# Performance work log

Hardware: AMD Instinct MI355X
Metric: run time of the kernel (lower is better)

## Reference

```python
import jax, jax.numpy as jnp
import numpy as np

NF = 51          # num_features = n_queries + 1
UNITS = 128      # rnn_units
LAG = 14
GAMMA = 28
OP_SCALE = 0.05
Q_SCALE = 0.02
C = float(np.log(np.expm1(1.0)))  # softplus shift so softplus(C)=1
OUT = 2 * NF     # DenseVariational units
NW = UNITS * OUT + OUT  # kernel + bias size = 13158


def setup_inputs() -> dict:
    key = jax.random.key(0)
    ks = jax.random.split(key, 6)
    B, T = 8192, 64
    x = jax.random.normal(ks[0], (B, T, NF), dtype=jnp.float32)
    gru_kernel = 0.1 * jax.random.normal(ks[1], (NF, 3 * UNITS), dtype=jnp.float32)
    gru_rkernel = 0.1 * jax.random.normal(ks[2], (UNITS, 3 * UNITS), dtype=jnp.float32)
    gru_bias = 0.05 * jax.random.normal(ks[3], (2, 3 * UNITS), dtype=jnp.float32)
    post_loc = 0.05 * jax.random.normal(ks[4], (NW,), dtype=jnp.float32)
    post_rho = -3.0 + 0.1 * jax.random.normal(ks[5], (NW,), dtype=jnp.float32)
    return {"x": x, "gru_kernel": gru_kernel, "gru_rkernel": gru_rkernel,
            "gru_bias": gru_bias, "post_loc": post_loc, "post_rho": post_rho}


def reference(x, gru_kernel, gru_rkernel, gru_bias, post_loc, post_rho):
    B = x.shape[0]

    def gru_step(h, xt):
        # Keras GRUCell, reset_after=True (dual bias)
        mx = xt @ gru_kernel + gru_bias[0]   # (B, 3U)
        mh = h @ gru_rkernel + gru_bias[1]   # (B, 3U)
        xz, xr, xh = jnp.split(mx, 3, axis=-1)
        rz, rr, rh = jnp.split(mh, 3, axis=-1)
        z = jax.nn.sigmoid(xz + rz)
        r = jax.nn.sigmoid(xr + rr)
        hh = jnp.tanh(xh + r * rh)
        return z * h + (1.0 - z) * hh

    def sample_dv(h, eps_w):
        # DenseVariational: sample flat weight vector from diag-Gaussian posterior
        scale = 1e-5 + Q_SCALE * jax.nn.softplus(C + post_rho)
        w = post_loc + scale * eps_w
        kernel = w[:UNITS * OUT].reshape(UNITS, OUT)
        bias = w[UNITS * OUT:]
        return h @ kernel + bias  # (B, OUT)

    # Deterministic sampling noise (reparameterization)
    nk = jax.random.key(42)
    eps_w = jax.random.normal(jax.random.fold_in(nk, 0), (GAMMA, NW), dtype=jnp.float32)
    eps_s = jax.random.normal(jax.random.fold_in(nk, 1), (GAMMA - 1, B, NF), dtype=jnp.float32)

    # Encoder GRU over inputs[:, :-LAG, :]
    seq = jnp.swapaxes(x[:, :-LAG, :], 0, 1)  # (T', B, NF)
    h0 = jnp.zeros((B, UNITS), dtype=x.dtype)
    h_enc = jax.lax.scan(lambda h, xt: (gru_step(h, xt), None), h0, seq)[0]

    t0 = sample_dv(h_enc, eps_w[0])  # (B, OUT)

    def dec_step(carry, eps):
        h, t = carry
        ew, es = eps
        loc = t[:, :NF]
        sc = 1e-5 + OP_SCALE * jax.nn.softplus(C + t[:, NF:])
        s = loc + sc * es                    # Normal(...).sample()
        h2 = gru_step(h, s)
        t2 = sample_dv(h2, ew)
        return (h2, t2), t2

    _, ts = jax.lax.scan(dec_step, (h_enc, t0), (eps_w[1:], eps_s))  # (GAMMA-1, B, OUT)
    preds = jnp.concatenate([t0[None], ts], axis=0)       # (GAMMA, B, OUT)
    preds = jnp.transpose(preds, (1, 0, 2))               # (B, GAMMA, OUT)

    loc = preds[..., :NF]
    scale = 1e-5 + OP_SCALE * jax.nn.softplus(C + preds[..., NF:])
    return jnp.concatenate([loc, scale], axis=-1)         # (B, GAMMA, 2*NF)
```

## Files before the change

### kernel.cpp

```cpp
#include <hip/hip_runtime.h>
#include <stdint.h>

#define NF 51
#define UNITS 128
#define G3 384
#define OUT_C 102
#define NW 13158
#define GAMMA 28
#define BATCH 8192
#define SEQ_T 64
#define TSTEPS 50
#define NDEC 27
#define BR 32
#define THREADS 1024
#define CCONST 0.5413248546129181f
#define WF_USHORTS 147456
#define WDF_USHORTS 802816
#define WDF_FRAG_THREADS 401408
#define HB_ELEMS 2856

typedef __attribute__((ext_vector_type(8))) short bf16x8;
typedef __attribute__((ext_vector_type(4))) float f32x4;
typedef unsigned short ushort_t;

__host__ __device__ __forceinline__ void tf2x32(uint32_t k0, uint32_t k1,
    uint32_t x0, uint32_t x1, uint32_t& o0, uint32_t& o1)
{
  uint32_t ks2 = k0 ^ k1 ^ 0x1BD11BDAu;
  x0 += k0; x1 += k1;
#define TF_R(r) { x0 += x1; x1 = (x1 << (r)) | (x1 >> (32 - (r))); x1 ^= x0; }
  TF_R(13) TF_R(15) TF_R(26) TF_R(6)  x0 += k1;  x1 += ks2 + 1u;
  TF_R(17) TF_R(29) TF_R(16) TF_R(24) x0 += ks2; x1 += k0 + 2u;
  TF_R(13) TF_R(15) TF_R(26) TF_R(6)  x0 += k0;  x1 += k1 + 3u;
  TF_R(17) TF_R(29) TF_R(16) TF_R(24) x0 += k1;  x1 += ks2 + 4u;
  TF_R(13) TF_R(15) TF_R(26) TF_R(6)  x0 += ks2; x1 += k0 + 5u;
#undef TF_R
  o0 = x0; o1 = x1;
}

__device__ __forceinline__ float erfinv_f(float x) {
  float w = -log1pf(-x * x);
  float p;
  if (w < 5.0f) {
    w -= 2.5f;
    p = 2.81022636e-08f;
    p = fmaf(p, w, 3.43273939e-07f);
    p = fmaf(p, w, -3.5233877e-06f);
    p = fmaf(p, w, -4.39150654e-06f);
    p = fmaf(p, w, 0.00021858087f);
    p = fmaf(p, w, -0.00125372503f);
    p = fmaf(p, w, -0.00417768164f);
    p = fmaf(p, w, 0.246640727f);
    p = fmaf(p, w, 1.50140941f);
  } else {
    w = sqrtf(w) - 3.0f;
    p = -0.000200214257f;
    p = fmaf(p, w, 0.000100950558f);
    p = fmaf(p, w, 0.00134934322f);
    p = fmaf(p, w, -0.00367342844f);
    p = fmaf(p, w, 0.00573950773f);
    p = fmaf(p, w, -0.0076224613f);
    p = fmaf(p, w, 0.00943887047f);
    p = fmaf(p, w, 1.00167406f);
    p = fmaf(p, w, 2.83297682f);
  }
  return p * x;
}

__device__ __forceinline__ float jax_normal(uint32_t k0, uint32_t k1, uint32_t i)
{
  uint32_t y0, y1;
  tf2x32(k0, k1, 0u, i, y0, y1);
  uint32_t bits = y0 ^ y1;
  uint32_t fb = (bits >> 9) | 0x3f800000u;
  float f = __uint_as_float(fb) - 1.0f;
  const float lo = -0.99999994f;
  const float d  = 1.99999994f;
  float u = __fadd_rn(__fmul_rn(f, d), lo);
  u = fmaxf(lo, u);
  return 1.41421354f * erfinv_f(u);
}

__device__ __forceinline__ float softplus_f(float x) {
  return fmaxf(x, 0.0f) + log1pf(expf(-fabsf(x)));
}
__device__ __forceinline__ float rcp_f(float x) { return __builtin_amdgcn_rcpf(x); }
__device__ __forceinline__ float sigmoid_fast(float x) {
  return rcp_f(1.0f + __expf(-x));
}
__device__ __forceinline__ float tanh_fast(float x) {
  return 1.0f - 2.0f * rcp_f(1.0f + __expf(2.0f * x));
}

__device__ __forceinline__ ushort_t f2bf(float f) {
  uint32_t u = __float_as_uint(f);
  uint32_t r = (u + 0x7fffu + ((u >> 16) & 1u)) >> 16;
  return (ushort_t)r;
}
__device__ __forceinline__ float bf2f(ushort_t h) {
  return __uint_as_float(((uint32_t)h) << 16);
}

__global__ void build_wf_kernel(const float* __restrict__ Wh,
                                const float* __restrict__ Wx,
                                ushort_t* __restrict__ wf)
{
  int t = blockIdx.x * 256 + threadIdx.x;
  if (t >= WF_USHORTS) return;
  int e    = t & 7;
  int lane = (t >> 3) & 63;
  int sp   = (t >> 9) & 1;
  int q    = t >> 10;
  int ks   = q % 6;
  int nb   = q / 6;
  int kl   = 8 * (lane >> 4) + e;
  int col  = 16 * nb + (lane & 15);
  float w;
  if (ks < 4) {
    w = Wh[(32 * ks + kl) * G3 + col];
  } else {
    int row = 32 * (ks - 4) + kl;
    w = (row < NF) ? Wx[row * G3 + col] : 0.0f;
  }
  ushort_t hi = f2bf(w);
  wf[t] = (sp == 0) ? hi : f2bf(w - bf2f(hi));
}

__global__ void build_wdf_kernel(const float* __restrict__ post_loc,
                                 const float* __restrict__ post_rho,
                                 ushort_t* __restrict__ wdf,
                                 float* __restrict__ hbias,
                                 uint32_t kw0, uint32_t kw1)
{
  int t = blockIdx.x * 256 + threadIdx.x;
  if (t < WDF_FRAG_THREADS) {
    int e    = t & 7;
    int lane = (t >> 3) & 63;
    int ks   = (t >> 9) & 3;
    int q    = t >> 11;
    int nt   = q % 7;
    int g    = q / 7;
    int k    = 32 * ks + 8 * (lane >> 4) + e;
    int col  = 16 * nt + (lane & 15);
    float w = 0.0f;
    if (col < OUT_C) {
      int widx = k * OUT_C + col;
      float eps = jax_normal(kw0, kw1, (uint32_t)(g * NW + widx));
      float sc = 1e-5f + 0.02f * softplus_f(CCONST + post_rho[widx]);
      w = fmaf(sc, eps, post_loc[widx]);
    }
    ushort_t hi = f2bf(w);
    size_t base = (size_t)(q * 4 + ks) * 1024 + lane * 8 + e;
    wdf[base]       = hi;
    wdf[base + 512] = f2bf(w - bf2f(hi));
  } else if (t < WDF_FRAG_THREADS + HB_ELEMS) {
    int u = t - WDF_FRAG_THREADS;
    int col = u % OUT_C, g = u / OUT_C;
    int widx = UNITS * OUT_C + col;
    float eps = jax_normal(kw0, kw1, (uint32_t)(g * NW + widx));
    float sc = 1e-5f + 0.02f * softplus_f(CCONST + post_rho[widx]);
    hbias[u] = fmaf(sc, eps, post_loc[widx]);
  }
}

__global__ __launch_bounds__(THREADS, 4)
__attribute__((amdgpu_waves_per_eu(4, 4)))
void irnn_main(
    const float* __restrict__ x,
    const float* __restrict__ gbias,
    const ushort_t* __restrict__ WF,
    const ushort_t* __restrict__ WDF,
    const float* __restrict__ HB,
    float* __restrict__ out,
    uint32_t ks0, uint32_t ks1)
{
  __shared__ __align__(16) ushort_t h_hi[BR][136];
  __shared__ __align__(16) ushort_t h_lo[BR][136];
  __shared__ __align__(16) ushort_t s_hi[BR][72];
  __shared__ __align__(16) ushort_t s_lo[BR][72];
  __shared__ float t_lds[BR][OUT_C];

  const int tid  = threadIdx.x;
  const int b0   = blockIdx.x * BR;
  const int lane = tid & 63;
  const int wv   = tid >> 6;
  const int kg   = lane >> 4;
  const int fr   = lane & 15;
  const int g3   = wv >> 1;
  const int rbase = 16 * (wv & 1);
  const int c    = 16 * g3 + fr;

  const float bz  = gbias[c]           + gbias[G3 + c];
  const float brg = gbias[UNITS + c]   + gbias[G3 + UNITS + c];
  const float bxh = gbias[2*UNITS + c];
  const float brh = gbias[G3 + 2*UNITS + c];

  float hreg[4] = {0.f, 0.f, 0.f, 0.f};

  for (int i = tid; i < BR * 136; i += THREADS) { (&h_hi[0][0])[i] = 0; (&h_lo[0][0])[i] = 0; }
  for (int i = tid; i < BR * 72;  i += THREADS) { (&s_hi[0][0])[i] = 0; (&s_lo[0][0])[i] = 0; }
  __syncthreads();

  const ushort_t* wfz = WF + (size_t)g3        * 6144 + (size_t)lane * 8;
  const ushort_t* wfr = WF + (size_t)(8 + g3)  * 6144 + (size_t)lane * 8;
  const ushort_t* wfh = WF + (size_t)(16 + g3) * 6144 + (size_t)lane * 8;

  auto gru_phase = [&]() {
    f32x4 acc_z  = {0.f,0.f,0.f,0.f};
    f32x4 acc_r  = {0.f,0.f,0.f,0.f};
    f32x4 acc_rh = {0.f,0.f,0.f,0.f};
    f32x4 acc_xh = {0.f,0.f,0.f,0.f};
    #pragma unroll 2
    for (int ks = 0; ks < 4; ++ks) {
      const int off = 32*ks + 8*kg;
      bf16x8 ah = *(const bf16x8*)&h_hi[rbase + fr][off];
      bf16x8 al = *(const bf16x8*)&h_lo[rbase + fr][off];
      bf16x8 bh = *(const bf16x8*)(wfz + (2*ks + 0) * 512);
      bf16x8 bl = *(const bf16x8*)(wfz + (2*ks + 1) * 512);
      acc_z = __builtin_amdgcn_mfma_f32_16x16x32_bf16(ah, bh, acc_z, 0,0,0);
      acc_z = __builtin_amdgcn_mfma_f32_16x16x32_bf16(ah, bl, acc_z, 0,0,0);
      acc_z = __builtin_amdgcn_mfma_f32_16x16x32_bf16(al, bh, acc_z, 0,0,0);
      bh = *(const bf16x8*)(wfr + (2*ks + 0) * 512);
      bl = *(const bf16x8*)(wfr + (2*ks + 1) * 512);
      acc_r = __builtin_amdgcn_mfma_f32_16x16x32_bf16(ah, bh, acc_r, 0,0,0);
      acc_r = __builtin_amdgcn_mfma_f32_16x16x32_bf16(ah, bl, acc_r, 0,0,0);
      acc_r = __builtin_amdgcn_mfma_f32_16x16x32_bf16(al, bh, acc_r, 0,0,0);
      bh = *(const bf16x8*)(wfh + (2*ks + 0) * 512);
      bl = *(const bf16x8*)(wfh + (2*ks + 1) * 512);
      acc_rh = __builtin_amdgcn_mfma_f32_16x16x32_bf16(ah, bh, acc_rh, 0,0,0);
      acc_rh = __builtin_amdgcn_mfma_f32_16x16x32_bf16(ah, bl, acc_rh, 0,0,0);
      acc_rh = __builtin_amdgcn_mfma_f32_16x16x32_bf16(al, bh, acc_rh, 0,0,0);
    }
    #pragma unroll 2
    for (int ks = 4; ks < 6; ++ks) {
      const int off = 32*(ks - 4) + 8*kg;
      bf16x8 ah = *(const bf16x8*)&s_hi[rbase + fr][off];
      bf16x8 al = *(const bf16x8*)&s_lo[rbase + fr][off];
      bf16x8 bh = *(const bf16x8*)(wfz + (2*ks + 0) * 512);
      bf16x8 bl = *(const bf16x8*)(wfz + (2*ks + 1) * 512);
      acc_z = __builtin_amdgcn_mfma_f32_16x16x32_bf16(ah, bh, acc_z, 0,0,0);
      acc_z = __builtin_amdgcn_mfma_f32_16x16x32_bf16(ah, bl, acc_z, 0,0,0);
      acc_z = __builtin_amdgcn_mfma_f32_16x16x32_bf16(al, bh, acc_z, 0,0,0);
      bh = *(const bf16x8*)(wfr + (2*ks + 0) * 512);
      bl = *(const bf16x8*)(wfr + (2*ks + 1) * 512);
      acc_r = __builtin_amdgcn_mfma_f32_16x16x32_bf16(ah, bh, acc_r, 0,0,0);
      acc_r = __builtin_amdgcn_mfma_f32_16x16x32_bf16(ah, bl, acc_r, 0,0,0);
      acc_r = __builtin_amdgcn_mfma_f32_16x16x32_bf16(al, bh, acc_r, 0,0,0);
      bh = *(const bf16x8*)(wfh + (2*ks + 0) * 512);
      bl = *(const bf16x8*)(wfh + (2*ks + 1) * 512);
      acc_xh = __builtin_amdgcn_mfma_f32_16x16x32_bf16(ah, bh, acc_xh, 0,0,0);
      acc_xh = __builtin_amdgcn_mfma_f32_16x16x32_bf16(ah, bl, acc_xh, 0,0,0);
      acc_xh = __builtin_amdgcn_mfma_f32_16x16x32_bf16(al, bh, acc_xh, 0,0,0);
    }
    __syncthreads();
    const int orow = rbase + 4 * kg;
    #pragma unroll
    for (int j = 0; j < 4; ++j) {
      float az = acc_z[j]  + bz;
      float ar = acc_r[j]  + brg;
      float rh = acc_rh[j] + brh;
      float xh = acc_xh[j] + bxh;
      float z  = sigmoid_fast(az);
      float rr = sigmoid_fast(ar);
      float hh = tanh_fast(fmaf(rr, rh, xh));
      float h  = z * hreg[j] + (1.0f - z) * hh;
      hreg[j]  = h;
      ushort_t hi = f2bf(h);
      h_hi[orow + j][c] = hi;
      h_lo[orow + j][c] = f2bf(h - bf2f(hi));
    }
  };

  auto head = [&](int g) {
    if (wv < 14) {
      const int nt = wv % 7, mt = wv / 7;
      const ushort_t* WB = WDF + (size_t)(g * 7 + nt) * 4096 + (size_t)lane * 8;
      f32x4 acc = {0.f,0.f,0.f,0.f};
      #pragma unroll 2
      for (int ks = 0; ks < 4; ++ks) {
        const int off = 32*ks + 8*kg;
        bf16x8 ah = *(const bf16x8*)&h_hi[16*mt + fr][off];
        bf16x8 al = *(const bf16x8*)&h_lo[16*mt + fr][off];
        bf16x8 bh = *(const bf16x8*)(WB + (2*ks + 0) * 512);
        bf16x8 bl = *(const bf16x8*)(WB + (2*ks + 1) * 512);
        acc = __builtin_amdgcn_mfma_f32_16x16x32_bf16(ah, bh, acc, 0,0,0);
        acc = __builtin_amdgcn_mfma_f32_16x16x32_bf16(ah, bl, acc, 0,0,0);
        acc = __builtin_amdgcn_mfma_f32_16x16x32_bf16(al, bh, acc, 0,0,0);
      }
      const int col = 16*nt + fr;
      if (col < OUT_C) {
        float kb = HB[g * OUT_C + col];
        const int r0 = 16*mt + 4*kg;
        #pragma unroll
        for (int j = 0; j < 4; ++j) {
          float tv = acc[j] + kb;
          t_lds[r0 + j][col] = tv;
          float ov = (col < NF) ? tv
                               : (1e-5f + 0.05f * softplus_f(CCONST + tv));
          out[(size_t)(b0 + r0 + j) * (GAMMA * OUT_C) + g * OUT_C + col] = ov;
        }
      }
    }
  };

  auto sphase = [&](int j) {
    for (int idx = tid; idx < BR * NF; idx += THREADS) {
      int r = idx / NF, f = idx - r * NF;
      float loc = t_lds[r][f];
      float sc = 1e-5f + 0.05f * softplus_f(CCONST + t_lds[r][NF + f]);
      uint32_t gi = (uint32_t)((j * BATCH + b0 + r) * NF + f);
      float es = jax_normal(ks0, ks1, gi);
      float s = fmaf(sc, es, loc);
      ushort_t hi = f2bf(s);
      s_hi[r][f] = hi;
      s_lo[r][f] = f2bf(s - bf2f(hi));
    }
  };

  for (int t = 0; t < TSTEPS; ++t) {
    for (int idx = tid; idx < BR * NF; idx += THREADS) {
      int r = idx / NF, f = idx - r * NF;
      float v = x[(size_t)(b0 + r) * (SEQ_T * NF) + t * NF + f];
      ushort_t hi = f2bf(v);
      s_hi[r][f] = hi;
      s_lo[r][f] = f2bf(v - bf2f(hi));
    }
    __syncthreads();
    gru_phase();
  }
  __syncthreads();
  head(0);
  __syncthreads();

  for (int j = 0; j < NDEC; ++j) {
    sphase(j);
    __syncthreads();
    gru_phase();
    __syncthreads();
    head(j + 1);
    __syncthreads();
  }
}

extern "C" void kernel_launch(void* const* d_in, const int* in_sizes, int n_in,
                              void* d_out, int out_size, void* d_ws, size_t ws_size,
                              hipStream_t stream)
{
  const float* x    = (const float*)d_in[0];
  const float* gk   = (const float*)d_in[1];
  const float* grk  = (const float*)d_in[2];
  const float* gb   = (const float*)d_in[3];
  const float* ploc = (const float*)d_in[4];
  const float* prho = (const float*)d_in[5];

  ushort_t* wf  = (ushort_t*)d_ws;
  ushort_t* wdf = wf + WF_USHORTS;
  float*    hb  = (float*)(wdf + WDF_USHORTS);

  uint32_t kw0, kw1, ksd0, ksd1;
  tf2x32(0u, 42u, 0u, 0u, kw0, kw1);
  tf2x32(0u, 42u, 0u, 1u, ksd0, ksd1);

  build_wf_kernel<<<(WF_USHORTS + 255) / 256, 256, 0, stream>>>(grk, gk, wf);
  build_wdf_kernel<<<(WDF_FRAG_THREADS + HB_ELEMS + 255) / 256, 256, 0, stream>>>(
      ploc, prho, wdf, hb, kw0, kw1);
  irnn_main<<<BATCH / BR, THREADS, 0, stream>>>(x, gb, wf, wdf, hb,
                                                (float*)d_out, ksd0, ksd1);
}
```

Before: 704.2 us.

## Warp-specialize GRU: 8 MFMA waves cover both row tiles, others prefetch next input

Each of the first 8 waves now computes the GRU gate GEMMs for both 16-row tiles, which reuses each loaded weight fragment twice and halves global weight reads per block. The other 8 waves load and split the next timestep's x into a double-buffered LDS input tile while the MFMA work runs, taking the input load off the critical path. The trade-off is that half the waves sit idle during the matmul, MFMA issue per step is serialized on fewer waves, and per-thread register pressure goes up from the doubled accumulators. A barrier is also added between the MFMA and combine phases.

```diff
diff --git a/kernel.cpp b/kernel.cpp
--- a/kernel.cpp
+++ b/kernel.cpp
@@ -176,8 +176,8 @@
 {
   __shared__ __align__(16) ushort_t h_hi[BR][136];
   __shared__ __align__(16) ushort_t h_lo[BR][136];
-  __shared__ __align__(16) ushort_t s_hi[BR][72];
-  __shared__ __align__(16) ushort_t s_lo[BR][72];
+  __shared__ __align__(16) ushort_t s_hi[2][BR][72];
+  __shared__ __align__(16) ushort_t s_lo[2][BR][72];
   __shared__ float t_lds[BR][OUT_C];
 
   const int tid  = threadIdx.x;
@@ -186,8 +186,7 @@
   const int wv   = tid >> 6;
   const int kg   = lane >> 4;
   const int fr   = lane & 15;
-  const int g3   = wv >> 1;
-  const int rbase = 16 * (wv & 1);
+  const int g3   = wv & 7;
   const int c    = 16 * g3 + fr;
 
   const float bz  = gbias[c]           + gbias[G3 + c];
@@ -195,79 +194,112 @@
   const float bxh = gbias[2*UNITS + c];
   const float brh = gbias[G3 + 2*UNITS + c];
 
-  float hreg[4] = {0.f, 0.f, 0.f, 0.f};
+  float hreg[8] = {0.f,0.f,0.f,0.f,0.f,0.f,0.f,0.f};
+  f32x4 cz[2], cr[2], crh[2], cxh[2];
 
   for (int i = tid; i < BR * 136; i += THREADS) { (&h_hi[0][0])[i] = 0; (&h_lo[0][0])[i] = 0; }
-  for (int i = tid; i < BR * 72;  i += THREADS) { (&s_hi[0][0])[i] = 0; (&s_lo[0][0])[i] = 0; }
+  for (int i = tid; i < 2 * BR * 72; i += THREADS) { (&s_hi[0][0][0])[i] = 0; (&s_lo[0][0][0])[i] = 0; }
   __syncthreads();
 
   const ushort_t* wfz = WF + (size_t)g3        * 6144 + (size_t)lane * 8;
   const ushort_t* wfr = WF + (size_t)(8 + g3)  * 6144 + (size_t)lane * 8;
   const ushort_t* wfh = WF + (size_t)(16 + g3) * 6144 + (size_t)lane * 8;
 
-  auto gru_phase = [&]() {
-    f32x4 acc_z  = {0.f,0.f,0.f,0.f};
-    f32x4 acc_r  = {0.f,0.f,0.f,0.f};
-    f32x4 acc_rh = {0.f,0.f,0.f,0.f};
-    f32x4 acc_xh = {0.f,0.f,0.f,0.f};
-    #pragma unroll 2
+  auto gru_mfma = [&](int buf) {
+    #pragma unroll
+    for (int m = 0; m < 2; ++m) {
+      cz[m]  = (f32x4){0.f,0.f,0.f,0.f};
+      cr[m]  = (f32x4){0.f,0.f,0.f,0.f};
+      crh[m] = (f32x4){0.f,0.f,0.f,0.f};
+      cxh[m] = (f32x4){0.f,0.f,0.f,0.f};
+    }
+    #pragma unroll 1
     for (int ks = 0; ks < 4; ++ks) {
       const int off = 32*ks + 8*kg;
-      bf16x8 ah = *(const bf16x8*)&h_hi[rbase + fr][off];
-      bf16x8 al = *(const bf16x8*)&h_lo[rbase + fr][off];
-      bf16x8 bh = *(const bf16x8*)(wfz + (2*ks + 0) * 512);
-      bf16x8 bl = *(const bf16x8*)(wfz + (2*ks + 1) * 512);
-      acc_z = __builtin_amdgcn_mfma_f32_16x16x32_bf16(ah, bh, acc_z, 0,0,0);
-      acc_z = __builtin_amdgcn_mfma_f32_16x16x32_bf16(ah, bl, acc_z, 0,0,0);
-      acc_z = __builtin_amdgcn_mfma_f32_16x16x32_bf16(al, bh, acc_z, 0,0,0);
-      bh = *(const bf16x8*)(wfr + (2*ks + 0) * 512);
-      bl = *(const bf16x8*)(wfr + (2*ks + 1) * 512);
-      acc_r = __builtin_amdgcn_mfma_f32_16x16x32_bf16(ah, bh, acc_r, 0,0,0);
-      acc_r = __builtin_amdgcn_mfma_f32_16x16x32_bf16(ah, bl, acc_r, 0,0,0);
-      acc_r = __builtin_amdgcn_mfma_f32_16x16x32_bf16(al, bh, acc_r, 0,0,0);
-      bh = *(const bf16x8*)(wfh + (2*ks + 0) * 512);
-      bl = *(const bf16x8*)(wfh + (2*ks + 1) * 512);
-      acc_rh = __builtin_amdgcn_mfma_f32_16x16x32_bf16(ah, bh, acc_rh, 0,0,0);
-      acc_rh = __builtin_amdgcn_mfma_f32_16x16x32_bf16(ah, bl, acc_rh, 0,0,0);
-      acc_rh = __builtin_amdgcn_mfma_f32_16x16x32_bf16(al, bh, acc_rh, 0,0,0);
-    }
-    #pragma unroll 2
+      bf16x8 ah[2], al[2];
+      ah[0] = *(const bf16x8*)&h_hi[fr][off];
+      al[0] = *(const bf16x8*)&h_lo[fr][off];
+      ah[1] = *(const bf16x8*)&h_hi[16 + fr][off];
+      al[1] = *(const bf16x8*)&h_lo[16 + fr][off];
+      bf16x8 bzh = *(const bf16x8*)(wfz + (2*ks + 0) * 512);
+      bf16x8 bzl = *(const bf16x8*)(wfz + (2*ks + 1) * 512);
+      bf16x8 brh_ = *(const bf16x8*)(wfr + (2*ks + 0) * 512);
+      bf16x8 brl_ = *(const bf16x8*)(wfr + (2*ks + 1) * 512);
+      bf16x8 bhh = *(const bf16x8*)(wfh + (2*ks + 0) * 512);
+      bf16x8 bhl = *(const bf16x8*)(wfh + (2*ks + 1) * 512);
+      #pragma unroll
+      for (int m = 0; m < 2; ++m) cz[m]  = __builtin_amdgcn_mfma_f32_16x16x32_bf16(ah[m], bzh, cz[m], 0,0,0);
+      #pragma unroll
+      for (int m = 0; m < 2; ++m) cr[m]  = __builtin_amdgcn_mfma_f32_16x16x32_bf16(ah[m], brh_, cr[m], 0,0,0);
+      #pragma unroll
+      for (int m = 0; m < 2; ++m) crh[m] = __builtin_amdgcn_mfma_f32_16x16x32_bf16(ah[m], bhh, crh[m], 0,0,0);
+      #pragma unroll
+      for (int m = 0; m < 2; ++m) cz[m]  = __builtin_amdgcn_mfma_f32_16x16x32_bf16(ah[m], bzl, cz[m], 0,0,0);
+      #pragma unroll
+      for (int m = 0; m < 2; ++m) cr[m]  = __builtin_amdgcn_mfma_f32_16x16x32_bf16(ah[m], brl_, cr[m], 0,0,0);
+      #pragma unroll
+      for (int m = 0; m < 2; ++m) crh[m] = __builtin_amdgcn_mfma_f32_16x16x32_bf16(ah[m], bhl, crh[m], 0,0,0);
+      #pragma unroll
+      for (int m = 0; m < 2; ++m) cz[m]  = __builtin_amdgcn_mfma_f32_16x16x32_bf16(al[m], bzh, cz[m], 0,0,0);
+      #pragma unroll
+      for (int m = 0; m < 2; ++m) cr[m]  = __builtin_amdgcn_mfma_f32_16x16x32_bf16(al[m], brh_, cr[m], 0,0,0);
+      #pragma unroll
+      for (int m = 0; m < 2; ++m) crh[m] = __builtin_amdgcn_mfma_f32_16x16x32_bf16(al[m], bhh, crh[m], 0,0,0);
+    }
+    #pragma unroll 1
     for (int ks = 4; ks < 6; ++ks) {
       const int off = 32*(ks - 4) + 8*kg;
-      bf16x8 ah = *(const bf16x8*)&s_hi[rbase + fr][off];
-      bf16x8 al = *(const bf16x8*)&s_lo[rbase + fr][off];
-      bf16x8 bh = *(const bf16x8*)(wfz + (2*ks + 0) * 512);
-      bf16x8 bl = *(const bf16x8*)(wfz + (2*ks + 1) * 512);
-      acc_z = __builtin_amdgcn_mfma_f32_16x16x32_bf16(ah, bh, acc_z, 0,0,0);
-      acc_z = __builtin_amdgcn_mfma_f32_16x16x32_bf16(ah, bl, acc_z, 0,0,0);
-      acc_z = __builtin_amdgcn_mfma_f32_16x16x32_bf16(al, bh, acc_z, 0,0,0);
-      bh = *(const bf16x8*)(wfr + (2*ks + 0) * 512);
-      bl = *(const bf16x8*)(wfr + (2*ks + 1) * 512);
-      acc_r = __builtin_amdgcn_mfma_f32_16x16x32_bf16(ah, bh, acc_r, 0,0,0);
-      acc_r = __builtin_amdgcn_mfma_f32_16x16x32_bf16(ah, bl, acc_r, 0,0,0);
-      acc_r = __builtin_amdgcn_mfma_f32_16x16x32_bf16(al, bh, acc_r, 0,0,0);
-      bh = *(const bf16x8*)(wfh + (2*ks + 0) * 512);
-      bl = *(const bf16x8*)(wfh + (2*ks + 1) * 512);
-      acc_xh = __builtin_amdgcn_mfma_f32_16x16x32_bf16(ah, bh, acc_xh, 0,0,0);
-      acc_xh = __builtin_amdgcn_mfma_f32_16x16x32_bf16(ah, bl, acc_xh, 0,0,0);
-      acc_xh = __builtin_amdgcn_mfma_f32_16x16x32_bf16(al, bh, acc_xh, 0,0,0);
-    }
-    __syncthreads();
-    const int orow = rbase + 4 * kg;
+      bf16x8 ah[2], al[2];
+      ah[0] = *(const bf16x8*)&s_hi[buf][fr][off];
+      al[0] = *(const bf16x8*)&s_lo[buf][fr][off];
+      ah[1] = *(const bf16x8*)&s_hi[buf][16 + fr][off];
+      al[1] = *(const bf16x8*)&s_lo[buf][16 + fr][off];
+      bf16x8 bzh = *(const bf16x8*)(wfz + (2*ks + 0) * 512);
+      bf16x8 bzl = *(const bf16x8*)(wfz + (2*ks + 1) * 512);
+      bf16x8 brh_ = *(const bf16x8*)(wfr + (2*ks + 0) * 512);
+      bf16x8 brl_ = *(const bf16x8*)(wfr + (2*ks + 1) * 512);
+      bf16x8 bhh = *(const bf16x8*)(wfh + (2*ks + 0) * 512);
+      bf16x8 bhl = *(const bf16x8*)(wfh + (2*ks + 1) * 512);
+      #pragma unroll
+      for (int m = 0; m < 2; ++m) cz[m]  = __builtin_amdgcn_mfma_f32_16x16x32_bf16(ah[m], bzh, cz[m], 0,0,0);
+      #pragma unroll
+      for (int m = 0; m < 2; ++m) cr[m]  = __builtin_amdgcn_mfma_f32_16x16x32_bf16(ah[m], brh_, cr[m], 0,0,0);
+      #pragma unroll
+      for (int m = 0; m < 2; ++m) cxh[m] = __builtin_amdgcn_mfma_f32_16x16x32_bf16(ah[m], bhh, cxh[m], 0,0,0);
+      #pragma unroll
+      for (int m = 0; m < 2; ++m) cz[m]  = __builtin_amdgcn_mfma_f32_16x16x32_bf16(ah[m], bzl, cz[m], 0,0,0);
+      #pragma unroll
+      for (int m = 0; m < 2; ++m) cr[m]  = __builtin_amdgcn_mfma_f32_16x16x32_bf16(ah[m], brl_, cr[m], 0,0,0);
+      #pragma unroll
+      for (int m = 0; m < 2; ++m) cxh[m] = __builtin_amdgcn_mfma_f32_16x16x32_bf16(ah[m], bhl, cxh[m], 0,0,0);
+      #pragma unroll
+      for (int m = 0; m < 2; ++m) cz[m]  = __builtin_amdgcn_mfma_f32_16x16x32_bf16(al[m], bzh, cz[m], 0,0,0);
+      #pragma unroll
+      for (int m = 0; m < 2; ++m) cr[m]  = __builtin_amdgcn_mfma_f32_16x16x32_bf16(al[m], brh_, cr[m], 0,0,0);
+      #pragma unroll
+      for (int m = 0; m < 2; ++m) cxh[m] = __builtin_amdgcn_mfma_f32_16x16x32_bf16(al[m], bhh, cxh[m], 0,0,0);
+    }
+  };
+
+  auto combine = [&]() {
     #pragma unroll
-    for (int j = 0; j < 4; ++j) {
-      float az = acc_z[j]  + bz;
-      float ar = acc_r[j]  + brg;
-      float rh = acc_rh[j] + brh;
-      float xh = acc_xh[j] + bxh;
-      float z  = sigmoid_fast(az);
-      float rr = sigmoid_fast(ar);
-      float hh = tanh_fast(fmaf(rr, rh, xh));
-      float h  = z * hreg[j] + (1.0f - z) * hh;
-      hreg[j]  = h;
-      ushort_t hi = f2bf(h);
-      h_hi[orow + j][c] = hi;
-      h_lo[orow + j][c] = f2bf(h - bf2f(hi));
+    for (int m = 0; m < 2; ++m) {
+      const int orow = 16*m + 4*kg;
+      #pragma unroll
+      for (int j = 0; j < 4; ++j) {
+        float az = cz[m][j]  + bz;
+        float ar = cr[m][j]  + brg;
+        float rh = crh[m][j] + brh;
+        float xh = cxh[m][j] + bxh;
+        float z  = sigmoid_fast(az);
+        float rr = sigmoid_fast(ar);
+        float hh = tanh_fast(fmaf(rr, rh, xh));
+        float h  = z * hreg[4*m + j] + (1.0f - z) * hh;
+        hreg[4*m + j] = h;
+        ushort_t hi = f2bf(h);
+        h_hi[orow + j][c] = hi;
+        h_lo[orow + j][c] = f2bf(h - bf2f(hi));
+      }
     }
   };
 
@@ -312,30 +344,45 @@
       float es = jax_normal(ks0, ks1, gi);
       float s = fmaf(sc, es, loc);
       ushort_t hi = f2bf(s);
-      s_hi[r][f] = hi;
-      s_lo[r][f] = f2bf(s - bf2f(hi));
+      s_hi[0][r][f] = hi;
+      s_lo[0][r][f] = f2bf(s - bf2f(hi));
     }
   };
 
+  for (int idx = tid; idx < BR * NF; idx += THREADS) {
+    int r = idx / NF, f = idx - r * NF;
+    float v = x[(size_t)(b0 + r) * (SEQ_T * NF) + f];
+    ushort_t hi = f2bf(v);
+    s_hi[0][r][f] = hi;
+    s_lo[0][r][f] = f2bf(v - bf2f(hi));
+  }
+  __syncthreads();
   for (int t = 0; t < TSTEPS; ++t) {
-    for (int idx = tid; idx < BR * NF; idx += THREADS) {
-      int r = idx / NF, f = idx - r * NF;
-      float v = x[(size_t)(b0 + r) * (SEQ_T * NF) + t * NF + f];
-      ushort_t hi = f2bf(v);
-      s_hi[r][f] = hi;
-      s_lo[r][f] = f2bf(v - bf2f(hi));
-    }
-    __syncthreads();
-    gru_phase();
-  }
-  __syncthreads();
+    if (wv < 8) {
+      gru_mfma(t & 1);
+    } else if (t + 1 < TSTEPS) {
+      const int nb = (t + 1) & 1;
+      for (int idx = tid - 512; idx < BR * NF; idx += 512) {
+        int r = idx / NF, f = idx - r * NF;
+        float v = x[(size_t)(b0 + r) * (SEQ_T * NF) + (t + 1) * NF + f];
+        ushort_t hi = f2bf(v);
+        s_hi[nb][r][f] = hi;
+        s_lo[nb][r][f] = f2bf(v - bf2f(hi));
+      }
+    }
+    __syncthreads();
+    if (wv < 8) combine();
+    __syncthreads();
+  }
   head(0);
   __syncthreads();
 
   for (int j = 0; j < NDEC; ++j) {
     sphase(j);
     __syncthreads();
-    gru_phase();
+    if (wv < 8) gru_mfma(0);
+    __syncthreads();
+    if (wv < 8) combine();
     __syncthreads();
     head(j + 1);
     __syncthreads();
```

Result: faster. 666.5 us (-5.4%).
